# Kernel optimization log

Hardware: AMD Instinct MI355X
Metric: run time of the kernel (lower is better)

## Reference

```python
import jax, jax.numpy as jnp
import numpy as np

NUM_HEADS, KEY_DIM, BLOCK, HALO = 8, 64, 8, 4
KV_KERNEL = BLOCK + 2 * HALO  # 16
EMB = NUM_HEADS * KEY_DIM     # 512


def setup_inputs() -> dict:
    key = jax.random.key(0)
    k = jax.random.split(key, 6)
    stddev = KEY_DIM ** -0.5
    return {
        "x": jax.random.normal(k[0], (8, 64, 64, 512), jnp.float32),
        "wq": jax.random.normal(k[1], (512, EMB), jnp.float32) * 0.02,
        "wkv": jax.random.normal(k[2], (512, 2 * EMB), jnp.float32) * 0.02,
        "wout": jax.random.normal(k[3], (EMB, EMB), jnp.float32) * 0.02,
        "pos_w": jax.random.normal(k[4], (KEY_DIM, 2 * KV_KERNEL - 1), jnp.float32) * stddev,
        "pos_h": jax.random.normal(k[5], (KEY_DIM, 2 * KV_KERNEL - 1), jnp.float32) * stddev,
    }


def rel_to_abs(rel):
    # rel: [B, N, hh, ww, 2*pos_dim-1] -> [B, N, hh, ww, pos_dim]
    b, n, hh, ww, dim = rel.shape
    pos_dim = (dim + 1) // 2
    gap = pos_dim - ww
    flat = rel.reshape(b, n, hh, ww * dim)[:, :, :, ww - 1:-1]
    return flat.reshape(b, n, hh, ww, 2 * (pos_dim - 1))[:, :, :, :, gap:pos_dim + gap]


def halo_forward(x, wq, wkv, wout, pos_w, pos_h):
    B, H, W, C = x.shape
    h, w = H // BLOCK, W // BLOCK
    K = KV_KERNEL
    scale = 1.0 / jnp.sqrt(jnp.asarray(KEY_DIM, x.dtype))

    # Query: [B, hd, h, w, block^2, key_dim]
    q = (x @ wq) * scale
    q = q.reshape(B, h, BLOCK, w, BLOCK, NUM_HEADS, KEY_DIM)
    attn_q = q.transpose(0, 5, 1, 3, 2, 4, 6).reshape(B, NUM_HEADS, h, w, BLOCK * BLOCK, KEY_DIM)

    # Overlapping halo KV windows (im2col-style gather, like tf.image.extract_patches)
    kv = x @ wkv
    kv_p = jnp.pad(kv, ((0, 0), (HALO, HALO), (HALO, HALO), (0, 0)))
    idx_h = jnp.arange(h)[:, None] * BLOCK + jnp.arange(K)[None, :]  # [h, K]
    idx_w = jnp.arange(w)[:, None] * BLOCK + jnp.arange(K)[None, :]  # [w, K]
    patches = kv_p[:, idx_h][:, :, :, idx_w]          # [B, h, K, w, K, 2*EMB]
    patches = patches.transpose(0, 1, 3, 2, 4, 5)     # [B, h, w, K, K, 2*EMB]
    patches = patches.reshape(B, h, w, K * K, NUM_HEADS, 2 * KEY_DIM)
    patches = patches.transpose(0, 4, 1, 2, 3, 5)     # [B, hd, h, w, K^2, 2*key_dim]
    key_t, val = patches[..., :KEY_DIM], patches[..., KEY_DIM:]

    scores = jnp.einsum('bnhwqc,bnhwkc->bnhwqk', attn_q, key_t)  # [B,hd,h,w,bq,bk]

    # Relative position logits (width + height), query already carries qk_scale
    pos_q = attn_q.reshape(B, NUM_HEADS * h * w, BLOCK, BLOCK, KEY_DIM)
    rel_w = rel_to_abs(pos_q @ pos_w)                                      # [B,N,hb,wb,K]
    rel_h = rel_to_abs(pos_q.transpose(0, 1, 3, 2, 4) @ pos_h)
    rel_h = rel_h.transpose(0, 1, 3, 2, 4)                                 # [B,N,hb,wb,K]
    pos = rel_w[..., None, :] + rel_h[..., :, None]                        # [B,N,hb,wb,Kh,Kw]
    pos = pos.reshape(B, NUM_HEADS, h, w, BLOCK * BLOCK, K * K)

    attn = jax.nn.softmax(scores + pos, axis=-1)
    out = jnp.einsum('bnhwqk,bnhwkc->bnhwqc', attn, val)
    out = out.reshape(B, NUM_HEADS, h, w, BLOCK, BLOCK, KEY_DIM)
    out = out.transpose(0, 2, 4, 3, 5, 1, 6).reshape(B, H, W, EMB)
    return out @ wout


def reference(x, wq, wkv, wout, pos_w, pos_h):
    return halo_forward(x, wq, wkv, wout, pos_w, pos_h)
```

## Files before the change

kernel.cpp:

```cpp
#include <hip/hip_runtime.h>
#include <hip/hip_fp16.h>
#include <math.h>

typedef _Float16 f16x8 __attribute__((ext_vector_type(8)));
typedef _Float16 f16x4 __attribute__((ext_vector_type(4)));
typedef float    f32x4 __attribute__((ext_vector_type(4)));

#define M_TOT 32768
#define VROW  4608
#define LOG2E 1.44269504088896f

__device__ __forceinline__ void gload16(const void* g, void* l) {
    __builtin_amdgcn_global_load_lds(
        (const __attribute__((address_space(1))) unsigned int*)g,
        (__attribute__((address_space(3))) unsigned int*)l, 16, 0, 0);
}

__device__ __forceinline__ f32x4 mfma32(f16x8 a, f16x8 b, f32x4 c) {
    return __builtin_amdgcn_mfma_f32_16x16x32_f16(a, b, c, 0, 0, 0);
}

__global__ __launch_bounds__(256) void prep(
    const float* __restrict__ x, const float* __restrict__ wq,
    const float* __restrict__ wkv, const float* __restrict__ wout,
    const float* __restrict__ posw, const float* __restrict__ posh,
    __half* __restrict__ x16, __half* __restrict__ wT, __half* __restrict__ woT,
    __half* __restrict__ posT, __half* __restrict__ vTp, __half* __restrict__ zp)
{
    const int bid = blockIdx.x, t = threadIdx.x;
    if (bid < 8192) {
        const size_t i = ((size_t)bid * 256 + t) * 8;
        float4 a = *(const float4*)&x[i];
        float4 b = *(const float4*)&x[i + 4];
        __half2 h[4];
        h[0] = __floats2half2_rn(a.x, a.y);
        h[1] = __floats2half2_rn(a.z, a.w);
        h[2] = __floats2half2_rn(b.x, b.y);
        h[3] = __floats2half2_rn(b.z, b.w);
        *(float4*)&x16[i] = *(float4*)h;
    } else if (bid < 12288) {
        const int id = (bid - 8192) * 256 + t;
        const int nr = id >> 9, k = id & 511;
        if (nr < 512) {
            wT[(size_t)nr * 512 + k] = __float2half(wq[k * 512 + nr] * (0.125f * LOG2E));
        } else if (nr < 1536) {
            wT[(size_t)nr * 512 + k] = __float2half(wkv[k * 1024 + (nr - 512)]);
        } else {
            woT[(size_t)(nr - 1536) * 512 + k] = __float2half(wout[k * 512 + (nr - 1536)]);
        }
    } else if (bid < 14336) {
        const int id = (bid - 12288) * 256 + t;
        const int row = id >> 7, rem = id & 127;
        const int y = rem >> 1, side = rem & 1;
        f16x4 z = {(_Float16)0.f, (_Float16)0.f, (_Float16)0.f, (_Float16)0.f};
        *(f16x4*)(vTp + (size_t)row * VROW + y * 72 + side * 68) = z;
    } else if (bid < 14352) {
        const int id = (bid - 14336) * 256 + t;
        const int tb = id >> 11, idx = (id >> 6) & 31, d = id & 63;
        const float* src = tb ? posh : posw;
        posT[id] = __float2half((idx < 31) ? src[d * 31 + idx] : 0.f);
    } else {
        if (t < 16) {
            float4 z = make_float4(0.f, 0.f, 0.f, 0.f);
            *(float4*)(zp + t * 8) = z;
        }
    }
}

template <int MODE, int NBN>
__global__ __launch_bounds__(256) void mfma_gemm(
    const __half* __restrict__ A, const __half* __restrict__ Bt,
    __half* __restrict__ q16, __half* __restrict__ k16, __half* __restrict__ vTp,
    float* __restrict__ outf)
{
    __shared__ __align__(16) char As[128 * 128];
    __shared__ __align__(16) char Bs[128 * 128];

    const int t = threadIdx.x;
    const int l = t & 63, w = t >> 6;
    const int wr = w >> 1, wc = w & 1;
    const int lr = l & 15, hi = l >> 4;

    const int bid = blockIdx.x;
    const int xcd = bid & 7, loc = bid >> 3;
    const int bm  = xcd * 32 + (loc & 31);
    const int bn  = loc >> 5;

    f32x4 acc[4][4];
    #pragma unroll
    for (int i = 0; i < 4; ++i)
        #pragma unroll
        for (int j = 0; j < 4; ++j) acc[i][j] = (f32x4){0.f, 0.f, 0.f, 0.f};

    const int sch = (t & 7);

    for (int k0 = 0; k0 < 512; k0 += 64) {
        #pragma unroll
        for (int it = 0; it < 4; ++it) {
            const int row = it * 32 + (t >> 3);
            const int kk  = k0 + ((sch ^ (row & 7)) * 8);
            gload16(A + (size_t)(bm * 128 + row) * 512 + kk,
                    As + (it * 256 + w * 64) * 16);
        }
        #pragma unroll
        for (int it = 0; it < 4; ++it) {
            const int row = it * 32 + (t >> 3);
            const int kk  = k0 + ((sch ^ (row & 7)) * 8);
            gload16(Bt + (size_t)(bn * 128 + row) * 512 + kk,
                    Bs + (it * 256 + w * 64) * 16);
        }
        __syncthreads();

        #pragma unroll
        for (int dc = 0; dc < 2; ++dc) {
            f16x8 af[4], bf[4];
            #pragma unroll
            for (int i = 0; i < 4; ++i) {
                const int ra = wr * 64 + i * 16 + lr;
                af[i] = *(const f16x8*)(As + ra * 128 + (((dc * 4 + hi) ^ (ra & 7)) * 16));
            }
            #pragma unroll
            for (int j = 0; j < 4; ++j) {
                const int rb = wc * 64 + j * 16 + lr;
                bf[j] = *(const f16x8*)(Bs + rb * 128 + (((dc * 4 + hi) ^ (rb & 7)) * 16));
            }
            #pragma unroll
            for (int i = 0; i < 4; ++i)
                #pragma unroll
                for (int j = 0; j < 4; ++j)
                    acc[i][j] = mfma32(af[i], bf[j], acc[i][j]);
        }
        __syncthreads();
    }

    const int lq = hi;
    #pragma unroll
    for (int i = 0; i < 4; ++i) {
        #pragma unroll
        for (int j = 0; j < 4; ++j) {
            const int row0 = bm * 128 + wr * 64 + i * 16 + lq * 4;
            const int col  = bn * 128 + wc * 64 + j * 16 + lr;
            if (MODE == 1) {
                #pragma unroll
                for (int r = 0; r < 4; ++r)
                    outf[(size_t)(row0 + r) * 512 + col] = acc[i][j][r];
            } else if (bn < 4) {
                #pragma unroll
                for (int r = 0; r < 4; ++r)
                    q16[(size_t)(row0 + r) * 512 + col] = __float2half(acc[i][j][r]);
            } else if (wc == 0) {
                const int head = bn - 4, d2 = j * 16 + lr;
                #pragma unroll
                for (int r = 0; r < 4; ++r)
                    k16[(size_t)(row0 + r) * 512 + head * 64 + d2] = __float2half(acc[i][j][r]);
            } else {
                const int head = bn - 4, d2 = j * 16 + lr;
                const int bb = row0 >> 12, pix = row0 & 4095;
                const int py = pix >> 6, px = pix & 63;
                f16x4 pv;
                #pragma unroll
                for (int r = 0; r < 4; ++r) pv[r] = (_Float16)acc[i][j][r];
                *(f16x4*)(vTp + ((size_t)((bb * 8 + head) * 64 + d2)) * VROW + py * 72 + px + 4) = pv;
            }
        }
    }
}

__global__ __launch_bounds__(256, 4) void halo_attn(
    const __half* __restrict__ qbuf, const __half* __restrict__ kbuf,
    const __half* __restrict__ vTp, const __half* __restrict__ posT,
    const __half* __restrict__ zp, __half* __restrict__ obuf)
{
    __shared__ __align__(16) char KP[64 * 520];
    __shared__ __align__(16) char POSB[6336];
    __shared__ float red[4][64];

    __half* RW = (__half*)POSB;
    __half* RH = (__half*)(POSB + 3168);
    float (*red2)[64] = (float(*)[64])POSB;

    const int hw = blockIdx.x;
    const int wg = (hw & 7) * 512 + (hw >> 3);
    const int wb = wg & 7, hb = (wg >> 3) & 7, n = (wg >> 6) & 7, b = wg >> 9;
    const int t = threadIdx.x;
    const int l = t & 63, g = t >> 6;
    const int hi = l >> 4, c15 = l & 15;

    #pragma unroll
    for (int it = 0; it < 8; ++it) {
        const int cid = it * 256 + t;
        const int S = cid * 16;
        const int row = S >> 7;
        const int d0h = (((S & 127) >> 4) ^ (row & 7)) * 8;
        const int ky = hb * 8 - 4 + (row >> 4);
        const int kx = wb * 8 - 4 + (row & 15);
        const bool ok = ((unsigned)ky < 64u) && ((unsigned)kx < 64u);
        const __half* src = ok ? (kbuf + ((size_t)((b * 64 + ky) * 64 + kx)) * 512 + n * 64 + d0h)
                               : zp;
        gload16(src, KP + (it * 256 + g * 64) * 16);
    }

    f16x8 vfrag[8];
    {
        const __half* vrow = vTp + ((size_t)((b * 8 + n) * 64 + g * 16 + c15)) * VROW;
        const int xoff = wb * 8 + (hi & 1) * 8;
        #pragma unroll
        for (int kc = 0; kc < 8; ++kc) {
            const int ki = kc * 2 + (hi >> 1);
            const int y = hb * 8 - 4 + ki;
            const __half* p = ((unsigned)y < 64u) ? (vrow + y * 72 + xoff) : zp;
            vfrag[kc] = *(const f16x8*)p;
        }
    }

    f16x8 qreg[4][2];
    #pragma unroll
    for (int qf = 0; qf < 4; ++qf) {
        const int q = qf * 16 + c15;
        const size_t pix = (size_t)((b * 64 + hb * 8 + (q >> 3)) * 64 + wb * 8 + (q & 7));
        #pragma unroll
        for (int dc = 0; dc < 2; ++dc)
            qreg[qf][dc] = *(const f16x8*)(qbuf + pix * 512 + n * 64 + dc * 32 + hi * 8);
    }

    {
        const int tb = g >> 1, ih = g & 1;
        f32x4 accp[4];
        #pragma unroll
        for (int qf = 0; qf < 4; ++qf) accp[qf] = (f32x4){0.f, 0.f, 0.f, 0.f};
        #pragma unroll
        for (int dc = 0; dc < 2; ++dc) {
            const f16x8 a = *(const f16x8*)(posT + tb * 2048 + (ih * 16 + c15) * 64 + dc * 32 + hi * 8);
            #pragma unroll
            for (int qf = 0; qf < 4; ++qf)
                accp[qf] = mfma32(a, qreg[qf][dc], accp[qf]);
        }
        __half* dst = tb ? RH : RW;
        #pragma unroll
        for (int qf = 0; qf < 4; ++qf)
            #pragma unroll
            for (int r = 0; r < 4; ++r) {
                const unsigned idx8 = (unsigned)(ih * 16 + hi * 4 + r) - 8u;
                if (idx8 < 23u)
                    dst[idx8 * 66 + qf * 16 + c15] = __float2half(accp[qf][r]);
            }
    }
    __syncthreads();

    f32x4 accs[4][4];
    #pragma unroll
    for (int kf = 0; kf < 4; ++kf)
        #pragma unroll
        for (int qf = 0; qf < 4; ++qf) accs[kf][qf] = (f32x4){0.f, 0.f, 0.f, 0.f};

    __builtin_amdgcn_s_setprio(1);
    #pragma unroll
    for (int kf = 0; kf < 4; ++kf) {
        const int row = g * 64 + kf * 16 + c15;
        #pragma unroll
        for (int dc = 0; dc < 2; ++dc) {
            const int off = (row * 128 + dc * 64 + hi * 16) ^ ((row & 7) << 4);
            f16x8 a = *(const f16x8*)(KP + off);
            #pragma unroll
            for (int qf = 0; qf < 4; ++qf)
                accs[kf][qf] = mfma32(a, qreg[qf][dc], accs[kf][qf]);
        }
    }
    __builtin_amdgcn_s_setprio(0);

    float mq[4];
    #pragma unroll
    for (int qf = 0; qf < 4; ++qf) {
        const int q = qf * 16 + c15;
        const int qj = q & 7, qi = q >> 3;
        float pa[4], pb[4];
        #pragma unroll
        for (int r = 0; r < 4; ++r)  pa[r] = __half2float(RW[(hi * 4 + r + 7 - qj) * 66 + q]);
        #pragma unroll
        for (int kf = 0; kf < 4; ++kf) pb[kf] = __half2float(RH[(g * 4 + kf + 7 - qi) * 66 + q]);
        float mm = -1e30f;
        #pragma unroll
        for (int kf = 0; kf < 4; ++kf)
            #pragma unroll
            for (int r = 0; r < 4; ++r) {
                const float s = accs[kf][qf][r] + pa[r] + pb[kf];
                accs[kf][qf][r] = s;
                mm = fmaxf(mm, s);
            }
        mm = fmaxf(mm, __shfl_xor(mm, 16));
        mm = fmaxf(mm, __shfl_xor(mm, 32));
        mq[qf] = mm;
    }
    if (l < 16) {
        #pragma unroll
        for (int qf = 0; qf < 4; ++qf) red[g][qf * 16 + l] = mq[qf];
    }
    __syncthreads();

    float sums[4];
    #pragma unroll
    for (int qf = 0; qf < 4; ++qf) {
        const int q = qf * 16 + c15;
        const float mfull = fmaxf(fmaxf(red[0][q], red[1][q]), fmaxf(red[2][q], red[3][q]));
        float ss = 0.f;
        #pragma unroll
        for (int kf = 0; kf < 4; ++kf)
            #pragma unroll
            for (int r = 0; r < 4; ++r) {
                const float p = exp2f(accs[kf][qf][r] - mfull);
                accs[kf][qf][r] = p;
                ss += p;
            }
        ss += __shfl_xor(ss, 16);
        ss += __shfl_xor(ss, 32);
        sums[qf] = ss;
        #pragma unroll
        for (int kf = 0; kf < 4; ++kf) {
            __half2 h01 = __floats2half2_rn(accs[kf][qf][0], accs[kf][qf][1]);
            __half2 h23 = __floats2half2_rn(accs[kf][qf][2], accs[kf][qf][3]);
            uint2 wv;
            wv.x = *(unsigned*)&h01;
            wv.y = *(unsigned*)&h23;
            *(uint2*)(KP + q * 520 + (g * 64 + kf * 16 + hi * 4) * 2) = wv;
        }
    }
    if (l < 16) {
        #pragma unroll
        for (int qf = 0; qf < 4; ++qf) red2[g][qf * 16 + l] = sums[qf];
    }
    __syncthreads();

    f32x4 acco[4];
    #pragma unroll
    for (int qf = 0; qf < 4; ++qf) acco[qf] = (f32x4){0.f, 0.f, 0.f, 0.f};
    __builtin_amdgcn_s_setprio(1);
    #pragma unroll
    for (int kc = 0; kc < 8; ++kc) {
        const f16x8 bf = vfrag[kc];
        #pragma unroll
        for (int qf = 0; qf < 4; ++qf) {
            const char* pp = KP + (qf * 16 + c15) * 520 + kc * 64 + hi * 16;
            const f16x4 p0 = *(const f16x4*)pp;
            const f16x4 p1 = *(const f16x4*)(pp + 8);
            const f16x8 af = __builtin_shufflevector(p0, p1, 0, 1, 2, 3, 4, 5, 6, 7);
            acco[qf] = mfma32(af, bf, acco[qf]);
        }
    }
    __builtin_amdgcn_s_setprio(0);

    #pragma unroll
    for (int qf = 0; qf < 4; ++qf) {
        #pragma unroll
        for (int r = 0; r < 4; ++r) {
            const int q = qf * 16 + hi * 4 + r;
            const float den = red2[0][q] + red2[1][q] + red2[2][q] + red2[3][q];
            const float v = acco[qf][r] * __builtin_amdgcn_rcpf(den);
            const size_t pix = (size_t)((b * 64 + hb * 8 + (q >> 3)) * 64 + wb * 8 + (q & 7));
            obuf[pix * 512 + n * 64 + g * 16 + c15] = __float2half(v);
        }
    }
}

extern "C" void kernel_launch(void* const* d_in, const int* in_sizes, int n_in,
                              void* d_out, int out_size, void* d_ws, size_t ws_size,
                              hipStream_t stream)
{
    const float* x    = (const float*)d_in[0];
    const float* wq   = (const float*)d_in[1];
    const float* wkv  = (const float*)d_in[2];
    const float* wout = (const float*)d_in[3];
    const float* posw = (const float*)d_in[4];
    const float* posh = (const float*)d_in[5];
    float* out = (float*)d_out;

    const size_t NPIX = (size_t)M_TOT * 512;
    const size_t NVTP = (size_t)64 * 64 * VROW;
    __half* x16  = (__half*)d_ws;
    __half* wT   = x16 + NPIX;
    __half* woT  = wT + (size_t)1536 * 512;
    __half* q16  = woT + (size_t)512 * 512;
    __half* k16  = q16 + NPIX;
    __half* vTp  = k16 + NPIX;
    __half* o16  = vTp + NVTP;
    __half* zp   = o16 + NPIX;
    __half* posT = zp + 128;

    prep<<<14353, 256, 0, stream>>>(x, wq, wkv, wout, posw, posh,
                                    x16, wT, woT, posT, vTp, zp);

    mfma_gemm<0, 12><<<3072, 256, 0, stream>>>(x16, wT, q16, k16, vTp, nullptr);

    halo_attn<<<4096, 256, 0, stream>>>(q16, k16, vTp, posT, zp, o16);

    mfma_gemm<1, 4><<<1024, 256, 0, stream>>>(o16, woT, nullptr, nullptr, nullptr, out);
}
```

Measured before the change: 215.0 us.

## Double-buffer GEMM LDS tiles and regroup block-to-tile mapping per XCD

Converts the projection GEMM's K loop to double-buffered LDS, issuing the global-to-LDS loads for the next K slice before running the MFMAs on the current one. A single waitcnt plus barrier per iteration replaces the two syncthreads. This is meant to hide global load latency behind compute. The block index mapping is also changed so that consecutive blocks on one XCD sweep 16 row tiles across all column tiles before moving on, which should improve L2 reuse of the A rows. The cost is twice the LDS per block, which may lower occupancy.

```diff
diff --git a/kernel.cpp b/kernel.cpp
--- a/kernel.cpp
+++ b/kernel.cpp
@@ -73,8 +73,8 @@
     __half* __restrict__ q16, __half* __restrict__ k16, __half* __restrict__ vTp,
     float* __restrict__ outf)
 {
-    __shared__ __align__(16) char As[128 * 128];
-    __shared__ __align__(16) char Bs[128 * 128];
+    __shared__ __align__(16) char As[2 * 16384];
+    __shared__ __align__(16) char Bs[2 * 16384];
 
     const int t = threadIdx.x;
     const int l = t & 63, w = t >> 6;
@@ -83,8 +83,10 @@
 
     const int bid = blockIdx.x;
     const int xcd = bid & 7, loc = bid >> 3;
-    const int bm  = xcd * 32 + (loc & 31);
-    const int bn  = loc >> 5;
+    const int half = loc / (16 * NBN);
+    const int rem  = loc % (16 * NBN);
+    const int bn   = rem >> 4;
+    const int bm   = xcd * 32 + half * 16 + (rem & 15);
 
     f32x4 acc[4][4];
     #pragma unroll
@@ -93,36 +95,48 @@
         for (int j = 0; j < 4; ++j) acc[i][j] = (f32x4){0.f, 0.f, 0.f, 0.f};
 
     const int sch = (t & 7);
-
-    for (int k0 = 0; k0 < 512; k0 += 64) {
+    const int srw = (t >> 3);
+
+    auto STAGE = [&](int sel, int k0) {
         #pragma unroll
         for (int it = 0; it < 4; ++it) {
-            const int row = it * 32 + (t >> 3);
+            const int row = it * 32 + srw;
             const int kk  = k0 + ((sch ^ (row & 7)) * 8);
             gload16(A + (size_t)(bm * 128 + row) * 512 + kk,
-                    As + (it * 256 + w * 64) * 16);
+                    As + sel * 16384 + (it * 256 + w * 64) * 16);
         }
         #pragma unroll
         for (int it = 0; it < 4; ++it) {
-            const int row = it * 32 + (t >> 3);
+            const int row = it * 32 + srw;
             const int kk  = k0 + ((sch ^ (row & 7)) * 8);
             gload16(Bt + (size_t)(bn * 128 + row) * 512 + kk,
-                    Bs + (it * 256 + w * 64) * 16);
-        }
-        __syncthreads();
-
+                    Bs + sel * 16384 + (it * 256 + w * 64) * 16);
+        }
+    };
+
+    STAGE(0, 0);
+    asm volatile("s_waitcnt vmcnt(0)" ::: "memory");
+    __builtin_amdgcn_s_barrier();
+
+    #pragma unroll
+    for (int k0 = 0; k0 < 512; k0 += 64) {
+        const int sel = (k0 >> 6) & 1;
+        if (k0 < 448) STAGE(sel ^ 1, k0 + 64);
+
+        const char* Ab = As + sel * 16384;
+        const char* Bb = Bs + sel * 16384;
         #pragma unroll
         for (int dc = 0; dc < 2; ++dc) {
             f16x8 af[4], bf[4];
             #pragma unroll
             for (int i = 0; i < 4; ++i) {
                 const int ra = wr * 64 + i * 16 + lr;
-                af[i] = *(const f16x8*)(As + ra * 128 + (((dc * 4 + hi) ^ (ra & 7)) * 16));
+                af[i] = *(const f16x8*)(Ab + ra * 128 + (((dc * 4 + hi) ^ (ra & 7)) * 16));
             }
             #pragma unroll
             for (int j = 0; j < 4; ++j) {
                 const int rb = wc * 64 + j * 16 + lr;
-                bf[j] = *(const f16x8*)(Bs + rb * 128 + (((dc * 4 + hi) ^ (rb & 7)) * 16));
+                bf[j] = *(const f16x8*)(Bb + rb * 128 + (((dc * 4 + hi) ^ (rb & 7)) * 16));
             }
             #pragma unroll
             for (int i = 0; i < 4; ++i)
@@ -130,7 +144,11 @@
                 for (int j = 0; j < 4; ++j)
                     acc[i][j] = mfma32(af[i], bf[j], acc[i][j]);
         }
-        __syncthreads();
+
+        if (k0 < 448) {
+            asm volatile("s_waitcnt vmcnt(0)" ::: "memory");
+            __builtin_amdgcn_s_barrier();
+        }
     }
 
     const int lq = hi;
```

Result: faster. 204.1 us (median of 3 runs) (-5.1%).
